# Kernel optimization log

Hardware: AMD Instinct MI355X
Metric: run time of the kernel (lower is better)

Reference implementation:

```python
import jax, jax.numpy as jnp
import numpy as np
from jax import lax

B, T, N, CIN, CH, COUT, K, KS, E = 2, 16, 2048, 32, 64, 64, 3, 3, 32768


def setup_inputs() -> dict:
    key = jax.random.key(0)
    ks = jax.random.split(key, 20)
    s = 0.05
    p = lambda k, shp: s * jax.random.normal(k, shp, dtype=jnp.float32)
    return {
        "X": jax.random.normal(ks[0], (B, T, N, CIN), dtype=jnp.float32),
        "edge_index": jax.random.randint(ks[1], (2, E), 0, N),
        "edge_weight": jax.random.uniform(ks[2], (E,), dtype=jnp.float32),
        "tc1_w1": p(ks[3], (CH, CIN, 1, KS)), "tc1_b1": p(ks[4], (CH,)),
        "tc1_w2": p(ks[5], (CH, CIN, 1, KS)), "tc1_b2": p(ks[6], (CH,)),
        "tc1_w3": p(ks[7], (CH, CIN, 1, KS)), "tc1_b3": p(ks[8], (CH,)),
        "cheb_w": p(ks[9], (K, CH, CH)), "cheb_b": p(ks[10], (CH,)),
        "tc2_w1": p(ks[11], (COUT, CH, 1, KS)), "tc2_b1": p(ks[12], (COUT,)),
        "tc2_w2": p(ks[13], (COUT, CH, 1, KS)), "tc2_b2": p(ks[14], (COUT,)),
        "tc2_w3": p(ks[15], (COUT, CH, 1, KS)), "tc2_b3": p(ks[16], (COUT,)),
        "bn_gamma": jnp.ones((N,), jnp.float32),
        "bn_beta": jnp.zeros((N,), jnp.float32),
    }


def _tconv(X, w1, b1, w2, b2, w3, b3):
    # X: (B, T, N, C) -> (B, C, N, T), gated temporal conv over last axis
    x = jnp.transpose(X, (0, 3, 2, 1))
    dn = ("NCHW", "OIHW", "NCHW")
    c = lambda w, b: lax.conv_general_dilated(x, w, (1, 1), "VALID", dimension_numbers=dn) + b[None, :, None, None]
    out = jax.nn.relu(c(w1, b1) + jax.nn.sigmoid(c(w2, b2)) + c(w3, b3))
    return jnp.transpose(out, (0, 3, 2, 1))


def _cheb(x, edge_index, edge_weight, W, b):
    # ChebConv, sym normalization, lambda_max=2 -> L_hat = -D^{-1/2} A D^{-1/2}
    row, col = edge_index[0], edge_index[1]
    w = jnp.where(row == col, 0.0, edge_weight)  # get_laplacian removes self-loops
    deg = jax.ops.segment_sum(w, row, num_segments=N)
    safe = jnp.where(deg > 0, deg, 1.0)
    dis = jnp.where(deg > 0, lax.rsqrt(safe), 0.0)
    norm = -dis[row] * w * dis[col]  # (E,)

    def prop(z):  # z: (B, T, N, C)
        zm = jnp.moveaxis(z, 2, 0)                      # (N, B, T, C)
        msg = zm[col] * norm[:, None, None, None]       # (E, B, T, C)
        agg = jax.ops.segment_sum(msg, row, num_segments=N)
        return jnp.moveaxis(agg, 0, 2)

    Tx0 = x
    out = jnp.einsum("btnc,co->btno", Tx0, W[0])
    Tx1 = prop(Tx0)
    out = out + jnp.einsum("btnc,co->btno", Tx1, W[1])
    for k in range(2, K):
        Tx2 = 2.0 * prop(Tx1) - Tx0
        out = out + jnp.einsum("btnc,co->btno", Tx2, W[k])
        Tx0, Tx1 = Tx1, Tx2
    return out + b


def reference(X, edge_index, edge_weight, tc1_w1, tc1_b1, tc1_w2, tc1_b2, tc1_w3, tc1_b3,
              cheb_w, cheb_b, tc2_w1, tc2_b1, tc2_w2, tc2_b2, tc2_w3, tc2_b3,
              bn_gamma, bn_beta):
    t1 = _tconv(X, tc1_w1, tc1_b1, tc1_w2, tc1_b2, tc1_w3, tc1_b3)   # (B, T-2, N, CH)
    t2 = jax.nn.relu(_cheb(t1, edge_index, edge_weight, cheb_w, cheb_b))
    t3 = _tconv(t2, tc2_w1, tc2_b1, tc2_w2, tc2_b2, tc2_w3, tc2_b3)  # (B, T-4, N, COUT)
    t = jnp.transpose(t3, (0, 2, 1, 3))  # (B, N, T', COUT): N is BN channel axis
    mu = jnp.mean(t, axis=(0, 2, 3), keepdims=True)
    var = jnp.var(t, axis=(0, 2, 3), keepdims=True)
    t = (t - mu) * lax.rsqrt(var + 1e-5) * bn_gamma[None, :, None, None] + bn_beta[None, :, None, None]
    return jnp.transpose(t, (0, 2, 1, 3))
```

## Files before the change

### kernel.cpp

```cpp
#include <hip/hip_runtime.h>
#include <cstdint>
#include <cstddef>

typedef unsigned short ushort_t;
typedef short bf16x8 __attribute__((ext_vector_type(8)));
typedef float f32x4 __attribute__((ext_vector_type(4)));

#define N_NODES 2048
#define E_EDGES 32768

constexpr int OFS_X     = 0;
constexpr int OFS_EW    = 2097152;
constexpr int OFS_SMALL = 2129920;
constexpr int SMALL_TOTAL = 72128;
constexpr int OFS_T1W1 = 2129920;
constexpr int OFS_T1B1 = 2136064;
constexpr int OFS_T1W2 = 2136128;
constexpr int OFS_T1B2 = 2142272;
constexpr int OFS_T1W3 = 2142336;
constexpr int OFS_T1B3 = 2148480;
constexpr int OFS_CHW  = 2148544;
constexpr int OFS_CHB  = 2160832;
constexpr int OFS_T2W1 = 2160896;
constexpr int OFS_T2B1 = 2173184;
constexpr int OFS_T2W2 = 2173248;
constexpr int OFS_T2B2 = 2185536;
constexpr int OFS_T2W3 = 2185600;
constexpr int OFS_T2B3 = 2197888;
constexpr int OFS_GAM  = 2197952;
constexpr int OFS_BET  = 2200000;
constexpr int CAN_TOTAL = 2202048;

__device__ __align__(16) ushort_t g_t1b [3670016];
__device__ __align__(16) ushort_t g_tx1b[3670016];
__device__ __align__(16) ushort_t g_tx2b[3670016];
__device__ __align__(16) ushort_t g_t2b [3670016];
__device__ __align__(16) float    g_t3 [3145728];
__device__ float    g_deg[N_NODES];
__device__ int      g_cnt[N_NODES];
__device__ int      g_cur[N_NODES];
__device__ float    g_scale[N_NODES];
__device__ float    g_shift[N_NODES];
__device__ __align__(8) int2 g_csrp[E_EDGES];
__device__ int      g_rowstart[N_NODES + 1];
__device__ __align__(16) ushort_t g_can[CAN_TOTAL];
__device__ __align__(16) ushort_t g_wb1[18432];
__device__ __align__(16) ushort_t g_wb2[36864];
__device__ __align__(16) ushort_t g_wbc[12288];

__device__ __forceinline__ float bfu(ushort_t u) { return __uint_as_float(((unsigned)u) << 16); }
__device__ __forceinline__ ushort_t f2bf(float f) {
    unsigned u = __float_as_uint(f);
    u = u + 0x7fffu + ((u >> 16) & 1u);
    return (ushort_t)(u >> 16);
}
#define BF16_ONES_PAIR 0x3F803F80u

__global__ void convert_big_kernel(const void* __restrict__ X, const void* __restrict__ ew,
                                   const unsigned* __restrict__ gam) {
    int idx = blockIdx.x * 256 + threadIdx.x;
    bool isbf = (gam[0] == BF16_ONES_PAIR);
    if (idx < N_NODES) { g_deg[idx] = 0.f; g_cnt[idx] = 0; g_cur[idx] = 0; }
    if (idx < 2097152) {
        g_can[idx] = isbf ? ((const ushort_t*)X)[idx] : f2bf(((const float*)X)[idx]);
    } else {
        int i = idx - 2097152;
        g_can[idx] = isbf ? ((const ushort_t*)ew)[i] : f2bf(((const float*)ew)[i]);
    }
}

struct SmallPtrs { const void* p[16]; };

__global__ void convert_small_kernel(SmallPtrs sp, const unsigned* __restrict__ gam) {
    const int sizes[16] = {6144, 64, 6144, 64, 6144, 64, 12288, 64,
                           12288, 64, 12288, 64, 12288, 64, 2048, 2048};
    int idx = blockIdx.x * 256 + threadIdx.x;
    if (idx >= SMALL_TOTAL) return;
    bool isbf = (gam[0] == BF16_ONES_PAIR);
    int j = 0, local = idx;
    while (local >= sizes[j]) { local -= sizes[j]; ++j; }
    const void* p = sp.p[j];
    g_can[OFS_SMALL + idx] = isbf ? ((const ushort_t*)p)[local]
                                  : f2bf(((const float*)p)[local]);
}

__global__ void repack_kernel() {
    int idx = blockIdx.x * 256 + threadIdx.x;
    if (idx < 18432) {
        int j = idx & 7, lane = (idx >> 3) & 63, kk = (idx >> 9) % 3;
        int nt = (idx / 1536) & 3, set = idx / 6144;
        int o = nt * 16 + (lane & 15);
        int k = kk * 32 + (lane >> 4) * 8 + j;
        int ci = k & 31, ks = k >> 5;
        int base = (set == 0) ? OFS_T1W1 : (set == 1) ? OFS_T1W2 : OFS_T1W3;
        g_wb1[idx] = g_can[base + o * 96 + ci * 3 + ks];
    } else if (idx < 18432 + 36864) {
        int t = idx - 18432;
        int j = t & 7, lane = (t >> 3) & 63, kk = (t >> 9) % 6;
        int nt = (t / 3072) & 3, set = t / 12288;
        int o = nt * 16 + (lane & 15);
        int k = kk * 32 + (lane >> 4) * 8 + j;
        int ci = k & 63, ks = k >> 6;
        int base = (set == 0) ? OFS_T2W1 : (set == 1) ? OFS_T2W2 : OFS_T2W3;
        g_wb2[t] = g_can[base + o * 192 + ci * 3 + ks];
    } else {
        int t = idx - 18432 - 36864;
        int j = t & 7, lane = (t >> 3) & 63, kk = (t >> 9) % 6;
        int nt = t / 3072;
        int o = nt * 16 + (lane & 15);
        int k = kk * 32 + (lane >> 4) * 8 + j;
        int sec = k >> 6, c = k & 63;
        g_wbc[t] = g_can[OFS_CHW + sec * 4096 + c * 64 + o];
    }
}

__global__ void edge_count_kernel(const int* __restrict__ ei) {
    int e = blockIdx.x * 256 + threadIdx.x;
    if (e >= E_EDGES) return;
    int r = ei[e];
    int c = ei[E_EDGES + e];
    float w = (r == c) ? 0.f : bfu(g_can[OFS_EW + e]);
    atomicAdd(&g_deg[r], w);
    atomicAdd(&g_cnt[r], 1);
}

__global__ void scan_kernel() {
    __shared__ int part[256];
    __shared__ int pre[256];
    int t = threadIdx.x;
    int base = t * 8;
    int s = 0;
#pragma unroll
    for (int i = 0; i < 8; ++i) s += g_cnt[base + i];
    part[t] = s;
    __syncthreads();
    if (t == 0) {
        int a = 0;
        for (int i = 0; i < 256; ++i) { pre[i] = a; a += part[i]; }
    }
    __syncthreads();
    int a = pre[t];
#pragma unroll
    for (int i = 0; i < 8; ++i) { g_rowstart[base + i] = a; a += g_cnt[base + i]; }
    if (t == 255) g_rowstart[N_NODES] = a;
}

__global__ void edge_scatter_kernel(const int* __restrict__ ei) {
    int e = blockIdx.x * 256 + threadIdx.x;
    if (e >= E_EDGES) return;
    int r = ei[e];
    int c = ei[E_EDGES + e];
    float w = (r == c) ? 0.f : bfu(g_can[OFS_EW + e]);
    float dr = g_deg[r], dc = g_deg[c];
    float nr = dr > 0.f ? rsqrtf(dr) : 0.f;
    float nc = dc > 0.f ? rsqrtf(dc) : 0.f;
    int pos = atomicAdd(&g_cur[r], 1);
    int at = g_rowstart[r] + pos;
    g_csrp[at] = make_int2(c, __float_as_int(-nr * w * nc));
}

template <int LAYER>
__global__ __launch_bounds__(256) void tconv_mfma_kernel() {
    constexpr int CIN_  = (LAYER == 1) ? 32 : 64;
    constexpr int T_in  = (LAYER == 1) ? 16 : 14;
    constexpr int T_out = (LAYER == 1) ? 14 : 12;
    constexpr int KST   = (CIN_ * 3) / 32;
    constexpr int PADK  = (LAYER == 1) ? 104 : 200;
    constexpr int OB1 = (LAYER == 1) ? OFS_T1B1 : OFS_T2B1;
    constexpr int OB2 = (LAYER == 1) ? OFS_T1B2 : OFS_T2B2;
    constexpr int OB3 = (LAYER == 1) ? OFS_T1B3 : OFS_T2B3;

    __shared__ ushort_t xs[64 * PADK];

    const int tid = threadIdx.x;
    const int lane = tid & 63;
    const int wv = tid >> 6;
    const int m0 = blockIdx.x * 64;
    const int n0 = m0 & (N_NODES - 1);
    const int s  = m0 >> 11;
    const int b  = s / T_out;
    const int t  = s - b * T_out;

#pragma unroll
    for (int ks = 0; ks < 3; ++ks) {
        if constexpr (LAYER == 1) {
            const ushort4* src = (const ushort4*)(g_can + OFS_X +
                ((size_t)(b * T_in + t + ks) * N_NODES + n0) * 32);
            for (int i = tid; i < 512; i += 256) {
                ushort4 v = src[i];
                int row = i >> 3, c4 = i & 7;
                *(ushort4*)&xs[row * PADK + ks * 32 + c4 * 4] = v;
            }
        } else {
            const ushort4* src = (const ushort4*)(g_t2b +
                ((size_t)(b * T_in + t + ks) * N_NODES + n0) * 64);
            for (int i = tid; i < 1024; i += 256) {
                ushort4 v = src[i];
                int row = i >> 4, c4 = i & 15;
                *(ushort4*)&xs[row * PADK + ks * 64 + c4 * 4] = v;
            }
        }
    }
    __syncthreads();

    const ushort_t* WB = (LAYER == 1) ? g_wb1 : g_wb2;
    f32x4 acc[3][4];
#pragma unroll
    for (int st = 0; st < 3; ++st)
#pragma unroll
        for (int nt = 0; nt < 4; ++nt) acc[st][nt] = (f32x4){0.f, 0.f, 0.f, 0.f};

    const int arow = wv * 16 + (lane & 15);
    const int kofs = (lane >> 4) * 8;
#pragma unroll
    for (int kk = 0; kk < KST; ++kk) {
        bf16x8 av = *(const bf16x8*)&xs[arow * PADK + kk * 32 + kofs];
#pragma unroll
        for (int st = 0; st < 3; ++st)
#pragma unroll
            for (int nt = 0; nt < 4; ++nt) {
                bf16x8 bv = ((const bf16x8*)WB)[((st * 4 + nt) * KST + kk) * 64 + lane];
                acc[st][nt] = __builtin_amdgcn_mfma_f32_16x16x32_bf16(av, bv, acc[st][nt], 0, 0, 0);
            }
    }

    const int col = lane & 15;
    const int quad = lane >> 4;
#pragma unroll
    for (int nt = 0; nt < 4; ++nt) {
        int o = nt * 16 + col;
        float b1 = bfu(g_can[OB1 + o]);
        float b2 = bfu(g_can[OB2 + o]);
        float b3 = bfu(g_can[OB3 + o]);
#pragma unroll
        for (int reg = 0; reg < 4; ++reg) {
            int m = m0 + wv * 16 + quad * 4 + reg;
            float q = acc[1][nt][reg] + b2;
            float v = (acc[0][nt][reg] + b1) + 1.f / (1.f + expf(-q)) + (acc[2][nt][reg] + b3);
            v = v > 0.f ? v : 0.f;
            if constexpr (LAYER == 1) g_t1b[(size_t)m * 64 + o] = f2bf(v);
            else                      g_t3 [(size_t)m * 64 + o] = v;
        }
    }
}

template <int MODE>
__global__ __launch_bounds__(256) void prop_kernel() {
    const ushort_t* __restrict__ src = (MODE == 0) ? g_t1b : g_tx1b;
    ushort_t* __restrict__ dst = (MODE == 0) ? g_tx1b : g_tx2b;
    const int n = blockIdx.x;
    const int c = threadIdx.x & 63;
    const int sg = threadIdx.x >> 6;
    const int beg = g_rowstart[n], end = g_rowstart[n + 1];
    const int s0 = sg * 7;

    float acc[7];
#pragma unroll
    for (int j = 0; j < 7; ++j) acc[j] = 0.f;

    int e = beg;
    for (; e + 2 <= end; e += 2) {
        int2 p0 = g_csrp[e];
        int2 p1 = g_csrp[e + 1];
        float w0 = __int_as_float(p0.y);
        float w1 = __int_as_float(p1.y);
        size_t b0 = ((size_t)p0.x << 6) + c;
        size_t b1 = ((size_t)p1.x << 6) + c;
#pragma unroll
        for (int j = 0; j < 7; ++j) {
            size_t so = (size_t)(s0 + j) * (N_NODES * 64);
            float v0 = bfu(src[so + b0]);
            float v1 = bfu(src[so + b1]);
            acc[j] = fmaf(w1, v1, fmaf(w0, v0, acc[j]));
        }
    }
    if (e < end) {
        int2 p0 = g_csrp[e];
        float w0 = __int_as_float(p0.y);
        size_t b0 = ((size_t)p0.x << 6) + c;
#pragma unroll
        for (int j = 0; j < 7; ++j)
            acc[j] = fmaf(w0, bfu(src[(size_t)(s0 + j) * (N_NODES * 64) + b0]), acc[j]);
    }

#pragma unroll
    for (int j = 0; j < 7; ++j) {
        size_t off = ((size_t)(s0 + j) * N_NODES + n) * 64 + c;
        if constexpr (MODE == 0) dst[off] = f2bf(acc[j]);
        else                     dst[off] = f2bf(2.f * acc[j] - bfu(g_t1b[off]));
    }
}

__global__ __launch_bounds__(256) void cheb_mfma_kernel() {
    constexpr int PADK = 200;
    __shared__ ushort_t xs[64 * PADK];

    const int tid = threadIdx.x;
    const int lane = tid & 63;
    const int wv = tid >> 6;
    const int m0 = blockIdx.x * 64;

#pragma unroll
    for (int sec = 0; sec < 3; ++sec) {
        const ushort_t* sp = (sec == 0) ? g_t1b : (sec == 1) ? g_tx1b : g_tx2b;
        const ushort4* src = (const ushort4*)(sp + (size_t)m0 * 64);
        for (int i = tid; i < 1024; i += 256) {
            ushort4 v = src[i];
            int row = i >> 4, c4 = i & 15;
            *(ushort4*)&xs[row * PADK + sec * 64 + c4 * 4] = v;
        }
    }
    __syncthreads();

    f32x4 acc[4];
#pragma unroll
    for (int nt = 0; nt < 4; ++nt) acc[nt] = (f32x4){0.f, 0.f, 0.f, 0.f};

    const int arow = wv * 16 + (lane & 15);
    const int kofs = (lane >> 4) * 8;
#pragma unroll
    for (int kk = 0; kk < 6; ++kk) {
        bf16x8 av = *(const bf16x8*)&xs[arow * PADK + kk * 32 + kofs];
#pragma unroll
        for (int nt = 0; nt < 4; ++nt) {
            bf16x8 bv = ((const bf16x8*)g_wbc)[(nt * 6 + kk) * 64 + lane];
            acc[nt] = __builtin_amdgcn_mfma_f32_16x16x32_bf16(av, bv, acc[nt], 0, 0, 0);
        }
    }

    const int col = lane & 15;
    const int quad = lane >> 4;
#pragma unroll
    for (int nt = 0; nt < 4; ++nt) {
        int o = nt * 16 + col;
        float bias = bfu(g_can[OFS_CHB + o]);
#pragma unroll
        for (int reg = 0; reg < 4; ++reg) {
            int m = m0 + wv * 16 + quad * 4 + reg;
            float v = acc[nt][reg] + bias;
            g_t2b[(size_t)m * 64 + o] = f2bf(v > 0.f ? v : 0.f);
        }
    }
}

__global__ __launch_bounds__(256) void bn_stats_kernel() {
    int n = blockIdx.x;
    int tid = threadIdx.x;
    int c = tid & 63;
    int sg = tid >> 6;
    float s1 = 0.f, s2 = 0.f;
    for (int s = sg; s < 24; s += 4) {
        float v = g_t3[((size_t)(s * N_NODES + n)) * 64 + c];
        s1 += v;
        s2 += v * v;
    }
    __shared__ float r1[256], r2[256];
    r1[tid] = s1;
    r2[tid] = s2;
    __syncthreads();
    for (int st = 128; st > 0; st >>= 1) {
        if (tid < st) { r1[tid] += r1[tid + st]; r2[tid] += r2[tid + st]; }
        __syncthreads();
    }
    if (tid == 0) {
        const float inv = 1.f / 1536.f;
        float mean = r1[0] * inv;
        float var  = r2[0] * inv - mean * mean;
        float rstd = rsqrtf(var + 1e-5f);
        float g = bfu(g_can[OFS_GAM + n]), be = bfu(g_can[OFS_BET + n]);
        g_scale[n] = rstd * g;
        g_shift[n] = be - mean * rstd * g;
    }
}

__global__ __launch_bounds__(256) void bn_apply_kernel(void* __restrict__ outp,
                                                       const unsigned* __restrict__ gam) {
    size_t i = (size_t)blockIdx.x * 256 + threadIdx.x;
    size_t e = i * 4;
    int n = (int)((e >> 6) & (N_NODES - 1));
    float4 v = *reinterpret_cast<const float4*>(g_t3 + e);
    float sc = g_scale[n], sh = g_shift[n];
    float r0 = v.x * sc + sh;
    float r1 = v.y * sc + sh;
    float r2 = v.z * sc + sh;
    float r3 = v.w * sc + sh;
    if (gam[0] == BF16_ONES_PAIR) {
        ushort4 ov;
        ov.x = f2bf(r0); ov.y = f2bf(r1); ov.z = f2bf(r2); ov.w = f2bf(r3);
        *reinterpret_cast<ushort4*>((ushort_t*)outp + e) = ov;
    } else {
        float4 ov = make_float4(r0, r1, r2, r3);
        *reinterpret_cast<float4*>((float*)outp + e) = ov;
    }
}

extern "C" void kernel_launch(void* const* d_in, const int* in_sizes, int n_in,
                              void* d_out, int out_size, void* d_ws, size_t ws_size,
                              hipStream_t stream) {
    const int* ei = (const int*)d_in[1];
    const unsigned* gam = (const unsigned*)d_in[17];

    convert_big_kernel<<<8320, 256, 0, stream>>>(d_in[0], d_in[2], gam);
    SmallPtrs sp;
    for (int i = 0; i < 16; ++i) sp.p[i] = d_in[3 + i];
    convert_small_kernel<<<(SMALL_TOTAL + 255) / 256, 256, 0, stream>>>(sp, gam);

    edge_count_kernel<<<E_EDGES / 256, 256, 0, stream>>>(ei);
    scan_kernel<<<1, 256, 0, stream>>>();
    edge_scatter_kernel<<<E_EDGES / 256, 256, 0, stream>>>(ei);

    repack_kernel<<<264, 256, 0, stream>>>();

    tconv_mfma_kernel<1><<<896, 256, 0, stream>>>();

    prop_kernel<0><<<N_NODES, 256, 0, stream>>>();
    prop_kernel<1><<<N_NODES, 256, 0, stream>>>();
    cheb_mfma_kernel<<<896, 256, 0, stream>>>();

    tconv_mfma_kernel<2><<<768, 256, 0, stream>>>();

    bn_stats_kernel<<<N_NODES, 256, 0, stream>>>();
    bn_apply_kernel<<<3072, 256, 0, stream>>>(d_out, gam);
}
```

Before: 197.2 us.

## Fuse BN stats into tconv2, merge setup kernels, vectorize prop gathers

Batch-norm statistics are now accumulated in the second temporal conv epilogue with wave shuffles and atomics, replacing the separate stats pass over t3. Setup work (edge counting, small-param conversion, CSR scatter, weight repack) is merged into fewer kernels that read raw inputs directly, and X conversion is skipped for bf16 inputs. The propagation kernel loads packed channel pairs and splits edges between half-waves, reducing the shuffle at the end. Atomic float accumulation makes the BN statistics order-dependent, so results are no longer bitwise deterministic.

```diff
diff --git a/kernel.cpp b/kernel.cpp
--- a/kernel.cpp
+++ b/kernel.cpp
@@ -10,22 +10,14 @@
 #define E_EDGES 32768
 
 constexpr int OFS_X     = 0;
-constexpr int OFS_EW    = 2097152;
 constexpr int OFS_SMALL = 2129920;
 constexpr int SMALL_TOTAL = 72128;
-constexpr int OFS_T1W1 = 2129920;
 constexpr int OFS_T1B1 = 2136064;
-constexpr int OFS_T1W2 = 2136128;
 constexpr int OFS_T1B2 = 2142272;
-constexpr int OFS_T1W3 = 2142336;
 constexpr int OFS_T1B3 = 2148480;
-constexpr int OFS_CHW  = 2148544;
 constexpr int OFS_CHB  = 2160832;
-constexpr int OFS_T2W1 = 2160896;
 constexpr int OFS_T2B1 = 2173184;
-constexpr int OFS_T2W2 = 2173248;
 constexpr int OFS_T2B2 = 2185536;
-constexpr int OFS_T2W3 = 2185600;
 constexpr int OFS_T2B3 = 2197888;
 constexpr int OFS_GAM  = 2197952;
 constexpr int OFS_BET  = 2200000;
@@ -39,6 +31,8 @@
 __device__ float    g_deg[N_NODES];
 __device__ int      g_cnt[N_NODES];
 __device__ int      g_cur[N_NODES];
+__device__ float    g_bnsum[N_NODES];
+__device__ float    g_bnsumsq[N_NODES];
 __device__ float    g_scale[N_NODES];
 __device__ float    g_shift[N_NODES];
 __device__ __align__(8) int2 g_csrp[E_EDGES];
@@ -49,51 +43,98 @@
 __device__ __align__(16) ushort_t g_wbc[12288];
 
 __device__ __forceinline__ float bfu(ushort_t u) { return __uint_as_float(((unsigned)u) << 16); }
+__device__ __forceinline__ float lo16(unsigned u) { return __uint_as_float(u << 16); }
+__device__ __forceinline__ float hi16(unsigned u) { return __uint_as_float(u & 0xffff0000u); }
 __device__ __forceinline__ ushort_t f2bf(float f) {
     unsigned u = __float_as_uint(f);
     u = u + 0x7fffu + ((u >> 16) & 1u);
     return (ushort_t)(u >> 16);
 }
+__device__ __forceinline__ float ldin(const void* p, int i, bool isbf) {
+    return isbf ? bfu(((const ushort_t*)p)[i]) : ((const float*)p)[i];
+}
 #define BF16_ONES_PAIR 0x3F803F80u
 
-__global__ void convert_big_kernel(const void* __restrict__ X, const void* __restrict__ ew,
-                                   const unsigned* __restrict__ gam) {
+__global__ void init_kernel(const void* __restrict__ X, const unsigned* __restrict__ gam) {
     int idx = blockIdx.x * 256 + threadIdx.x;
+    if (idx < N_NODES) {
+        g_deg[idx] = 0.f; g_cnt[idx] = 0; g_cur[idx] = 0;
+        g_bnsum[idx] = 0.f; g_bnsumsq[idx] = 0.f;
+    }
     bool isbf = (gam[0] == BF16_ONES_PAIR);
-    if (idx < N_NODES) { g_deg[idx] = 0.f; g_cnt[idx] = 0; g_cur[idx] = 0; }
-    if (idx < 2097152) {
-        g_can[idx] = isbf ? ((const ushort_t*)X)[idx] : f2bf(((const float*)X)[idx]);
+    if (!isbf) g_can[OFS_X + idx] = f2bf(((const float*)X)[idx]);
+}
+
+struct SmallPtrs { const void* p[16]; };
+struct WPtrs { const void* p[7]; };
+
+__global__ void setup_a_kernel(const int* __restrict__ ei, const void* __restrict__ ew,
+                               SmallPtrs sp, const unsigned* __restrict__ gam) {
+    bool isbf = (gam[0] == BF16_ONES_PAIR);
+    int blk = blockIdx.x;
+    if (blk < 128) {
+        int e = blk * 256 + threadIdx.x;
+        int r = ei[e];
+        int c = ei[E_EDGES + e];
+        float w = (r == c) ? 0.f : ldin(ew, e, isbf);
+        atomicAdd(&g_deg[r], w);
+        atomicAdd(&g_cnt[r], 1);
     } else {
-        int i = idx - 2097152;
-        g_can[idx] = isbf ? ((const ushort_t*)ew)[i] : f2bf(((const float*)ew)[i]);
-    }
-}
-
-struct SmallPtrs { const void* p[16]; };
-
-__global__ void convert_small_kernel(SmallPtrs sp, const unsigned* __restrict__ gam) {
-    const int sizes[16] = {6144, 64, 6144, 64, 6144, 64, 12288, 64,
-                           12288, 64, 12288, 64, 12288, 64, 2048, 2048};
-    int idx = blockIdx.x * 256 + threadIdx.x;
-    if (idx >= SMALL_TOTAL) return;
+        const int sizes[16] = {6144, 64, 6144, 64, 6144, 64, 12288, 64,
+                               12288, 64, 12288, 64, 12288, 64, 2048, 2048};
+        int idx = (blk - 128) * 256 + threadIdx.x;
+        if (idx >= SMALL_TOTAL) return;
+        int j = 0, local = idx;
+        while (local >= sizes[j]) { local -= sizes[j]; ++j; }
+        g_can[OFS_SMALL + idx] = f2bf(ldin(sp.p[j], local, isbf));
+    }
+}
+
+__global__ void scan_kernel() {
+    __shared__ int part[256];
+    __shared__ int pre[256];
+    int t = threadIdx.x;
+    int base = t * 8;
+    int s = 0;
+#pragma unroll
+    for (int i = 0; i < 8; ++i) s += g_cnt[base + i];
+    part[t] = s;
+    __syncthreads();
+    if (t == 0) {
+        int a = 0;
+        for (int i = 0; i < 256; ++i) { pre[i] = a; a += part[i]; }
+    }
+    __syncthreads();
+    int a = pre[t];
+#pragma unroll
+    for (int i = 0; i < 8; ++i) { g_rowstart[base + i] = a; a += g_cnt[base + i]; }
+    if (t == 255) g_rowstart[N_NODES] = a;
+}
+
+__global__ void setup_b_kernel(const int* __restrict__ ei, const void* __restrict__ ew,
+                               WPtrs wp, const unsigned* __restrict__ gam) {
     bool isbf = (gam[0] == BF16_ONES_PAIR);
-    int j = 0, local = idx;
-    while (local >= sizes[j]) { local -= sizes[j]; ++j; }
-    const void* p = sp.p[j];
-    g_can[OFS_SMALL + idx] = isbf ? ((const ushort_t*)p)[local]
-                                  : f2bf(((const float*)p)[local]);
-}
-
-__global__ void repack_kernel() {
-    int idx = blockIdx.x * 256 + threadIdx.x;
+    int blk = blockIdx.x;
+    if (blk < 128) {
+        int e = blk * 256 + threadIdx.x;
+        int r = ei[e];
+        int c = ei[E_EDGES + e];
+        float w = (r == c) ? 0.f : ldin(ew, e, isbf);
+        float dr = g_deg[r], dc = g_deg[c];
+        float nr = dr > 0.f ? rsqrtf(dr) : 0.f;
+        float nc = dc > 0.f ? rsqrtf(dc) : 0.f;
+        int pos = atomicAdd(&g_cur[r], 1);
+        g_csrp[g_rowstart[r] + pos] = make_int2(c, __float_as_int(-nr * w * nc));
+        return;
+    }
+    int idx = (blk - 128) * 256 + threadIdx.x;
     if (idx < 18432) {
         int j = idx & 7, lane = (idx >> 3) & 63, kk = (idx >> 9) % 3;
         int nt = (idx / 1536) & 3, set = idx / 6144;
         int o = nt * 16 + (lane & 15);
         int k = kk * 32 + (lane >> 4) * 8 + j;
         int ci = k & 31, ks = k >> 5;
-        int base = (set == 0) ? OFS_T1W1 : (set == 1) ? OFS_T1W2 : OFS_T1W3;
-        g_wb1[idx] = g_can[base + o * 96 + ci * 3 + ks];
+        g_wb1[idx] = f2bf(ldin(wp.p[set], o * 96 + ci * 3 + ks, isbf));
     } else if (idx < 18432 + 36864) {
         int t = idx - 18432;
         int j = t & 7, lane = (t >> 3) & 63, kk = (t >> 9) % 6;
@@ -101,8 +142,7 @@
         int o = nt * 16 + (lane & 15);
         int k = kk * 32 + (lane >> 4) * 8 + j;
         int ci = k & 63, ks = k >> 6;
-        int base = (set == 0) ? OFS_T2W1 : (set == 1) ? OFS_T2W2 : OFS_T2W3;
-        g_wb2[t] = g_can[base + o * 192 + ci * 3 + ks];
+        g_wb2[t] = f2bf(ldin(wp.p[3 + set], o * 192 + ci * 3 + ks, isbf));
     } else {
         int t = idx - 18432 - 36864;
         int j = t & 7, lane = (t >> 3) & 63, kk = (t >> 9) % 6;
@@ -110,57 +150,13 @@
         int o = nt * 16 + (lane & 15);
         int k = kk * 32 + (lane >> 4) * 8 + j;
         int sec = k >> 6, c = k & 63;
-        g_wbc[t] = g_can[OFS_CHW + sec * 4096 + c * 64 + o];
-    }
-}
-
-__global__ void edge_count_kernel(const int* __restrict__ ei) {
-    int e = blockIdx.x * 256 + threadIdx.x;
-    if (e >= E_EDGES) return;
-    int r = ei[e];
-    int c = ei[E_EDGES + e];
-    float w = (r == c) ? 0.f : bfu(g_can[OFS_EW + e]);
-    atomicAdd(&g_deg[r], w);
-    atomicAdd(&g_cnt[r], 1);
-}
-
-__global__ void scan_kernel() {
-    __shared__ int part[256];
-    __shared__ int pre[256];
-    int t = threadIdx.x;
-    int base = t * 8;
-    int s = 0;
-#pragma unroll
-    for (int i = 0; i < 8; ++i) s += g_cnt[base + i];
-    part[t] = s;
-    __syncthreads();
-    if (t == 0) {
-        int a = 0;
-        for (int i = 0; i < 256; ++i) { pre[i] = a; a += part[i]; }
-    }
-    __syncthreads();
-    int a = pre[t];
-#pragma unroll
-    for (int i = 0; i < 8; ++i) { g_rowstart[base + i] = a; a += g_cnt[base + i]; }
-    if (t == 255) g_rowstart[N_NODES] = a;
-}
-
-__global__ void edge_scatter_kernel(const int* __restrict__ ei) {
-    int e = blockIdx.x * 256 + threadIdx.x;
-    if (e >= E_EDGES) return;
-    int r = ei[e];
-    int c = ei[E_EDGES + e];
-    float w = (r == c) ? 0.f : bfu(g_can[OFS_EW + e]);
-    float dr = g_deg[r], dc = g_deg[c];
-    float nr = dr > 0.f ? rsqrtf(dr) : 0.f;
-    float nc = dc > 0.f ? rsqrtf(dc) : 0.f;
-    int pos = atomicAdd(&g_cur[r], 1);
-    int at = g_rowstart[r] + pos;
-    g_csrp[at] = make_int2(c, __float_as_int(-nr * w * nc));
+        g_wbc[t] = f2bf(ldin(wp.p[6], sec * 4096 + c * 64 + o, isbf));
+    }
 }
 
 template <int LAYER>
-__global__ __launch_bounds__(256) void tconv_mfma_kernel() {
+__global__ __launch_bounds__(256) void tconv_mfma_kernel(const void* __restrict__ Xraw,
+                                                         const unsigned* __restrict__ gam) {
     constexpr int CIN_  = (LAYER == 1) ? 32 : 64;
     constexpr int T_in  = (LAYER == 1) ? 16 : 14;
     constexpr int T_out = (LAYER == 1) ? 14 : 12;
@@ -184,7 +180,9 @@
 #pragma unroll
     for (int ks = 0; ks < 3; ++ks) {
         if constexpr (LAYER == 1) {
-            const ushort4* src = (const ushort4*)(g_can + OFS_X +
+            bool isbf = (gam[0] == BF16_ONES_PAIR);
+            const ushort_t* xsrc = isbf ? (const ushort_t*)Xraw : (g_can + OFS_X);
+            const ushort4* src = (const ushort4*)(xsrc +
                 ((size_t)(b * T_in + t + ks) * N_NODES + n0) * 32);
             for (int i = tid; i < 512; i += 256) {
                 ushort4 v = src[i];
@@ -226,6 +224,8 @@
 
     const int col = lane & 15;
     const int quad = lane >> 4;
+    float rs1[4] = {0.f, 0.f, 0.f, 0.f};
+    float rs2[4] = {0.f, 0.f, 0.f, 0.f};
 #pragma unroll
     for (int nt = 0; nt < 4; ++nt) {
         int o = nt * 16 + col;
@@ -238,56 +238,86 @@
             float q = acc[1][nt][reg] + b2;
             float v = (acc[0][nt][reg] + b1) + 1.f / (1.f + expf(-q)) + (acc[2][nt][reg] + b3);
             v = v > 0.f ? v : 0.f;
-            if constexpr (LAYER == 1) g_t1b[(size_t)m * 64 + o] = f2bf(v);
-            else                      g_t3 [(size_t)m * 64 + o] = v;
+            if constexpr (LAYER == 1) {
+                g_t1b[(size_t)m * 64 + o] = f2bf(v);
+            } else {
+                g_t3[(size_t)m * 64 + o] = v;
+                rs1[reg] += v;
+                rs2[reg] += v * v;
+            }
+        }
+    }
+    if constexpr (LAYER == 2) {
+#pragma unroll
+        for (int reg = 0; reg < 4; ++reg) {
+            float s1 = rs1[reg], s2 = rs2[reg];
+#pragma unroll
+            for (int msk = 1; msk < 16; msk <<= 1) {
+                s1 += __shfl_xor(s1, msk, 64);
+                s2 += __shfl_xor(s2, msk, 64);
+            }
+            if (col == 0) {
+                int n = n0 + wv * 16 + quad * 4 + reg;
+                atomicAdd(&g_bnsum[n], s1);
+                atomicAdd(&g_bnsumsq[n], s2);
+            }
         }
     }
 }
 
 template <int MODE>
 __global__ __launch_bounds__(256) void prop_kernel() {
-    const ushort_t* __restrict__ src = (MODE == 0) ? g_t1b : g_tx1b;
-    ushort_t* __restrict__ dst = (MODE == 0) ? g_tx1b : g_tx2b;
+    const unsigned* __restrict__ srcu =
+        (const unsigned*)((MODE == 0) ? g_t1b : g_tx1b);
+    unsigned* __restrict__ dstu = (unsigned*)((MODE == 0) ? g_tx1b : g_tx2b);
     const int n = blockIdx.x;
-    const int c = threadIdx.x & 63;
+    const int lane = threadIdx.x & 63;
     const int sg = threadIdx.x >> 6;
-    const int beg = g_rowstart[n], end = g_rowstart[n + 1];
+    const int h = lane >> 5;
+    const int c2 = lane & 31;
+    const int beg = g_rowstart[n];
+    const int nE = g_rowstart[n + 1] - beg;
     const int s0 = sg * 7;
 
-    float acc[7];
-#pragma unroll
-    for (int j = 0; j < 7; ++j) acc[j] = 0.f;
-
-    int e = beg;
-    for (; e + 2 <= end; e += 2) {
-        int2 p0 = g_csrp[e];
-        int2 p1 = g_csrp[e + 1];
-        float w0 = __int_as_float(p0.y);
-        float w1 = __int_as_float(p1.y);
-        size_t b0 = ((size_t)p0.x << 6) + c;
-        size_t b1 = ((size_t)p1.x << 6) + c;
+    float a0[7], a1[7];
+#pragma unroll
+    for (int j = 0; j < 7; ++j) { a0[j] = 0.f; a1[j] = 0.f; }
+
+    for (int i = 0; i < nE; i += 4) {
+        int ia = i + h, ib = i + 2 + h;
+        bool va = ia < nE, vb = ib < nE;
+        int2 pa = g_csrp[beg + (va ? ia : 0)];
+        int2 pb = g_csrp[beg + (vb ? ib : 0)];
+        float wa = va ? __int_as_float(pa.y) : 0.f;
+        float wb = vb ? __int_as_float(pb.y) : 0.f;
+        unsigned ba = ((unsigned)pa.x << 5) + c2;
+        unsigned bb = ((unsigned)pb.x << 5) + c2;
 #pragma unroll
         for (int j = 0; j < 7; ++j) {
-            size_t so = (size_t)(s0 + j) * (N_NODES * 64);
-            float v0 = bfu(src[so + b0]);
-            float v1 = bfu(src[so + b1]);
-            acc[j] = fmaf(w1, v1, fmaf(w0, v0, acc[j]));
-        }
-    }
-    if (e < end) {
-        int2 p0 = g_csrp[e];
-        float w0 = __int_as_float(p0.y);
-        size_t b0 = ((size_t)p0.x << 6) + c;
-#pragma unroll
-        for (int j = 0; j < 7; ++j)
-            acc[j] = fmaf(w0, bfu(src[(size_t)(s0 + j) * (N_NODES * 64) + b0]), acc[j]);
-    }
-
+            size_t so = (size_t)(s0 + j) * (N_NODES * 32);
+            unsigned ua = srcu[so + ba];
+            unsigned ub = srcu[so + bb];
+            a0[j] = fmaf(wb, lo16(ub), fmaf(wa, lo16(ua), a0[j]));
+            a1[j] = fmaf(wb, hi16(ub), fmaf(wa, hi16(ua), a1[j]));
+        }
+    }
 #pragma unroll
     for (int j = 0; j < 7; ++j) {
-        size_t off = ((size_t)(s0 + j) * N_NODES + n) * 64 + c;
-        if constexpr (MODE == 0) dst[off] = f2bf(acc[j]);
-        else                     dst[off] = f2bf(2.f * acc[j] - bfu(g_t1b[off]));
+        a0[j] += __shfl_xor(a0[j], 32, 64);
+        a1[j] += __shfl_xor(a1[j], 32, 64);
+    }
+    if (h == 0) {
+#pragma unroll
+        for (int j = 0; j < 7; ++j) {
+            size_t off = ((size_t)(s0 + j) * N_NODES + n) * 32 + c2;
+            float v0 = a0[j], v1 = a1[j];
+            if constexpr (MODE == 1) {
+                unsigned tv = ((const unsigned*)g_t1b)[off];
+                v0 = 2.f * v0 - lo16(tv);
+                v1 = 2.f * v1 - hi16(tv);
+            }
+            dstu[off] = (unsigned)f2bf(v0) | ((unsigned)f2bf(v1) << 16);
+        }
     }
 }
 
@@ -343,34 +373,16 @@
     }
 }
 
-__global__ __launch_bounds__(256) void bn_stats_kernel() {
-    int n = blockIdx.x;
-    int tid = threadIdx.x;
-    int c = tid & 63;
-    int sg = tid >> 6;
-    float s1 = 0.f, s2 = 0.f;
-    for (int s = sg; s < 24; s += 4) {
-        float v = g_t3[((size_t)(s * N_NODES + n)) * 64 + c];
-        s1 += v;
-        s2 += v * v;
-    }
-    __shared__ float r1[256], r2[256];
-    r1[tid] = s1;
-    r2[tid] = s2;
-    __syncthreads();
-    for (int st = 128; st > 0; st >>= 1) {
-        if (tid < st) { r1[tid] += r1[tid + st]; r2[tid] += r2[tid + st]; }
-        __syncthreads();
-    }
-    if (tid == 0) {
-        const float inv = 1.f / 1536.f;
-        float mean = r1[0] * inv;
-        float var  = r2[0] * inv - mean * mean;
-        float rstd = rsqrtf(var + 1e-5f);
-        float g = bfu(g_can[OFS_GAM + n]), be = bfu(g_can[OFS_BET + n]);
-        g_scale[n] = rstd * g;
-        g_shift[n] = be - mean * rstd * g;
-    }
+__global__ void bn_finalize_kernel() {
+    int n = blockIdx.x * 256 + threadIdx.x;
+    if (n >= N_NODES) return;
+    const float inv = 1.f / 1536.f;
+    float mean = g_bnsum[n] * inv;
+    float var  = g_bnsumsq[n] * inv - mean * mean;
+    float rstd = rsqrtf(var + 1e-5f);
+    float g = bfu(g_can[OFS_GAM + n]), be = bfu(g_can[OFS_BET + n]);
+    g_scale[n] = rstd * g;
+    g_shift[n] = be - mean * rstd * g;
 }
 
 __global__ __launch_bounds__(256) void bn_apply_kernel(void* __restrict__ outp,
@@ -397,28 +409,31 @@
 extern "C" void kernel_launch(void* const* d_in, const int* in_sizes, int n_in,
                               void* d_out, int out_size, void* d_ws, size_t ws_size,
                               hipStream_t stream) {
+    const void* X = d_in[0];
     const int* ei = (const int*)d_in[1];
+    const void* ew = d_in[2];
     const unsigned* gam = (const unsigned*)d_in[17];
 
-    convert_big_kernel<<<8320, 256, 0, stream>>>(d_in[0], d_in[2], gam);
     SmallPtrs sp;
     for (int i = 0; i < 16; ++i) sp.p[i] = d_in[3 + i];
-    convert_small_kernel<<<(SMALL_TOTAL + 255) / 256, 256, 0, stream>>>(sp, gam);
-
-    edge_count_kernel<<<E_EDGES / 256, 256, 0, stream>>>(ei);
+    WPtrs wp;
+    wp.p[0] = d_in[3];  wp.p[1] = d_in[5];  wp.p[2] = d_in[7];
+    wp.p[3] = d_in[11]; wp.p[4] = d_in[13]; wp.p[5] = d_in[15];
+    wp.p[6] = d_in[9];
+
+    init_kernel<<<8192, 256, 0, stream>>>(X, gam);
+    setup_a_kernel<<<410, 256, 0, stream>>>(ei, ew, sp, gam);
     scan_kernel<<<1, 256, 0, stream>>>();
-    edge_scatter_kernel<<<E_EDGES / 256, 256, 0, stream>>>(ei);
-
-    repack_kernel<<<264, 256, 0, stream>>>();
-
-    tconv_mfma_kernel<1><<<896, 256, 0, stream>>>();
+    setup_b_kernel<<<392, 256, 0, stream>>>(ei, ew, wp, gam);
+
+    tconv_mfma_kernel<1><<<896, 256, 0, stream>>>(X, gam);
 
     prop_kernel<0><<<N_NODES, 256, 0, stream>>>();
     prop_kernel<1><<<N_NODES, 256, 0, stream>>>();
     cheb_mfma_kernel<<<896, 256, 0, stream>>>();
 
-    tconv_mfma_kernel<2><<<768, 256, 0, stream>>>();
-
-    bn_stats_kernel<<<N_NODES, 256, 0, stream>>>();
+    tconv_mfma_kernel<2><<<768, 256, 0, stream>>>(X, gam);
+
+    bn_finalize_kernel<<<8, 256, 0, stream>>>();
     bn_apply_kernel<<<3072, 256, 0, stream>>>(d_out, gam);
 }
```

After: 223.5 us. 1.13x slower.
